# Performance work log

Hardware: AMD Instinct MI355X
Metric: run time of the kernel (lower is better)

## Reference

```python
import jax, jax.numpy as jnp
import numpy as np

N_NODES = 100000
N_EDGES = 1000000
N_GRAPHS = 5000
H = 64
F_IN = 14  # QM9 num_features (11) + pos (3)
BN_EPS = 1e-5


def setup_inputs() -> dict:
    key = jax.random.key(0)
    ks = jax.random.split(key, 16)

    def w(k, shape, fan_in):
        return (jax.random.normal(k, shape, jnp.float32) / np.sqrt(fan_in)).astype(jnp.float32)

    inp = {
        "x": jax.random.normal(ks[0], (N_NODES, 11), jnp.float32),
        "pos": jax.random.normal(ks[1], (N_NODES, 3), jnp.float32),
        "edge_index": jax.random.randint(ks[2], (2, N_EDGES), 0, N_NODES, dtype=jnp.int32),
        "batch": jnp.sort(jax.random.randint(ks[3], (N_NODES,), 0, N_GRAPHS, dtype=jnp.int32)),
    }
    dims = [F_IN, H, H]
    i = 4
    for l, din in enumerate(dims, 1):
        inp[f"w{l}a"] = w(ks[i], (din, H), din); i += 1
        inp[f"b{l}a"] = jnp.zeros((H,), jnp.float32)
        inp[f"g{l}"] = jnp.ones((H,), jnp.float32)   # BatchNorm gamma
        inp[f"be{l}"] = jnp.zeros((H,), jnp.float32)  # BatchNorm beta
        inp[f"w{l}b"] = w(ks[i], (H, H), H); i += 1
        inp[f"b{l}b"] = jnp.zeros((H,), jnp.float32)
    inp["wl1"] = w(ks[i], (3 * H, H), 3 * H); i += 1
    inp["bl1"] = jnp.zeros((H,), jnp.float32)
    inp["wl2"] = w(ks[i], (H, 1), H)
    inp["bl2"] = jnp.zeros((1,), jnp.float32)
    return inp


def _gin_layer(x, src, dst, w1, b1, g, be, w2, b2):
    # GINConv (eps=0): h = MLP(x + sum_{j in N(i)} x_j)
    agg = jax.ops.segment_sum(x[src], dst, num_segments=x.shape[0])
    h = (x + agg) @ w1 + b1
    # BatchNorm1d in training mode: batch stats over node dim (biased var)
    mu = jnp.mean(h, axis=0)
    var = jnp.mean((h - mu) ** 2, axis=0)
    h = jax.nn.relu(g * (h - mu) * jax.lax.rsqrt(var + BN_EPS) + be)
    return jax.nn.relu(h @ w2 + b2)


def _mean_pool(x, batch):
    s = jax.ops.segment_sum(x, batch, num_segments=N_GRAPHS)
    c = jax.ops.segment_sum(jnp.ones((x.shape[0], 1), x.dtype), batch, num_segments=N_GRAPHS)
    return s / jnp.maximum(c, 1.0)


def reference(x, pos, edge_index, batch,
              w1a, b1a, g1, be1, w1b, b1b,
              w2a, b2a, g2, be2, w2b, b2b,
              w3a, b3a, g3, be3, w3b, b3b,
              wl1, bl1, wl2, bl2):
    src, dst = edge_index[0], edge_index[1]
    h0 = jnp.concatenate([x, pos], axis=1)                 # [N, 14]
    x1 = _gin_layer(h0, src, dst, w1a, b1a, g1, be1, w1b, b1b)
    x2 = _gin_layer(x1, src, dst, w2a, b2a, g2, be2, w2b, b2b)
    x3 = _gin_layer(x2, src, dst, w3a, b3a, g3, be3, w3b, b3b)
    p = jnp.concatenate([_mean_pool(x1, batch), _mean_pool(x2, batch), _mean_pool(x3, batch)], axis=1)  # [G, 192]
    h = jax.nn.relu(p @ wl1 + bl1)
    return h @ wl2 + bl2                                   # [G, 1]
```

## Files before the change

### kernel.cpp

```cpp
#include <hip/hip_runtime.h>
#include <hip/hip_bf16.h>

#define BN_EPS 1e-5f
#define LDP 132
#define LDS_BF 72
#define BSH 9
#define EPB 4096

typedef short bf16x8 __attribute__((ext_vector_type(8)));
typedef float f32x4 __attribute__((ext_vector_type(4)));

__device__ __forceinline__ float loadf(const void* p, long long i, unsigned bf) {
    if (bf) return __bfloat162float(((const __hip_bfloat16*)p)[i]);
    return ((const float*)p)[i];
}
__device__ __forceinline__ float b2f(unsigned short u) {
    return __uint_as_float(((unsigned)u) << 16);
}
__device__ __forceinline__ unsigned short f2b(float f) {
    __hip_bfloat16 h = __float2bfloat16(f);
    return *(unsigned short*)&h;
}
__device__ __forceinline__ float blo(unsigned u) { return __uint_as_float(u << 16); }
__device__ __forceinline__ float bhi(unsigned u) { return __uint_as_float(u & 0xffff0000u); }

__global__ void k_detect(const unsigned* g1w, unsigned* flag) {
    if (threadIdx.x == 0) *flag = (*g1w == 0x3F803F80u) ? 1u : 0u;
}

struct Srcs { const void* p[22]; };

__global__ void k_convert(Srcs s, const unsigned* flag, float* dst) {
    const int sizes[22] = {896,64,64,64,4096,64,  4096,64,64,64,4096,64,
                           4096,64,64,64,4096,64, 12288,64,64,1};
    const int offs[22]  = {0,896,960,1024,1088,5184, 5248,9344,9408,9472,9536,13632,
                           13696,17792,17856,17920,17984,22080, 22144,34432,34496,34560};
    int t = blockIdx.x;
    unsigned bf = *flag;
    const void* src = s.p[t];
    float* d = dst + offs[t];
    int n = sizes[t];
    for (int i = threadIdx.x; i < n; i += blockDim.x) d[i] = loadf(src, i, bf);
}

__global__ __launch_bounds__(256) void k_build(const void* x, const void* pos, const int* batch,
                        const unsigned* flag, unsigned short* h0b, float* cnt, int N) {
    int i = blockIdx.x * blockDim.x + threadIdx.x;
    if (i >= N) return;
    unsigned bf = *flag;
    unsigned short v[16];
    #pragma unroll
    for (int k = 0; k < 11; k++) v[k] = f2b(loadf(x, (long long)i * 11 + k, bf));
    #pragma unroll
    for (int k = 0; k < 3; k++) v[11 + k] = f2b(loadf(pos, (long long)i * 3 + k, bf));
    v[14] = 0; v[15] = 0;
    #pragma unroll
    for (int k = 0; k < 4; k++)
        *(ushort4*)&h0b[(long long)i * 16 + k * 4] = make_ushort4(v[4*k], v[4*k+1], v[4*k+2], v[4*k+3]);
    atomicAdd(&cnt[batch[i]], 1.0f);
}

__global__ __launch_bounds__(256) void k_bhist(const int* __restrict__ ei, int* __restrict__ bcnt,
                                               int E, int NCH, int NBK) {
    __shared__ int h[1024];
    int c = blockIdx.x, t = threadIdx.x;
    for (int i = t; i < NBK; i += 256) h[i] = 0;
    __syncthreads();
    int base = c * EPB;
    for (int i = t; i < EPB; i += 256) {
        int e = base + i;
        if (e < E) atomicAdd(&h[ei[E + e] >> BSH], 1);
    }
    __syncthreads();
    for (int i = t; i < NBK; i += 256) bcnt[i * NCH + c] = h[i];
}

__global__ __launch_bounds__(256) void k_scan_partial(const int* __restrict__ src, int* partial, int M) {
    __shared__ int sr[4];
    int b = blockIdx.x, t = threadIdx.x;
    int base = b * 1024;
    int s = 0;
    #pragma unroll
    for (int k = 0; k < 4; k++) {
        int i = base + k * 256 + t;
        if (i < M) s += src[i];
    }
    #pragma unroll
    for (int off = 32; off; off >>= 1) s += __shfl_down(s, off);
    if ((t & 63) == 0) sr[t >> 6] = s;
    __syncthreads();
    if (t == 0) partial[b] = sr[0] + sr[1] + sr[2] + sr[3];
}

__global__ __launch_bounds__(1024) void k_scan_chunks(const int* partial, int* chunkoff, int nchunks) {
    __shared__ int sp[1024];
    int t = threadIdx.x;
    sp[t] = (t < nchunks) ? partial[t] : 0;
    __syncthreads();
    for (int off = 1; off < 1024; off <<= 1) {
        int v = (t >= off) ? sp[t - off] : 0;
        __syncthreads();
        sp[t] += v;
        __syncthreads();
    }
    if (t < nchunks) chunkoff[t] = (t == 0) ? 0 : sp[t - 1];
}

__global__ __launch_bounds__(256) void k_scan_final(const int* __restrict__ src, const int* chunkoff,
                                                    int* __restrict__ out, int M) {
    __shared__ int sp[256];
    int b = blockIdx.x, t = threadIdx.x;
    int base = b * 1024 + t * 4;
    int v0 = 0, v1 = 0, v2 = 0, v3 = 0;
    if (base + 0 < M) v0 = src[base + 0];
    if (base + 1 < M) v1 = src[base + 1];
    if (base + 2 < M) v2 = src[base + 2];
    if (base + 3 < M) v3 = src[base + 3];
    int s = v0 + v1 + v2 + v3;
    sp[t] = s;
    __syncthreads();
    for (int off = 1; off < 256; off <<= 1) {
        int v = (t >= off) ? sp[t - off] : 0;
        __syncthreads();
        sp[t] += v;
        __syncthreads();
    }
    int run = chunkoff[b] + sp[t] - s;
    if (base + 0 < M) { out[base + 0] = run; run += v0; }
    if (base + 1 < M) { out[base + 1] = run; run += v1; }
    if (base + 2 < M) { out[base + 2] = run; run += v2; }
    if (base + 3 < M) { out[base + 3] = run; }
}

__global__ __launch_bounds__(256) void k_place(const int* __restrict__ ei, const int* __restrict__ boff,
                                               int2* __restrict__ ebuf, int E, int NCH, int NBK) {
    __shared__ int cur[1024];
    int c = blockIdx.x, t = threadIdx.x;
    for (int i = t; i < NBK; i += 256) cur[i] = boff[i * NCH + c];
    __syncthreads();
    int base = c * EPB;
    for (int i = t; i < EPB; i += 256) {
        int e = base + i;
        if (e < E) {
            int s = ei[e], d = ei[E + e];
            int pos = atomicAdd(&cur[d >> BSH], 1);
            ebuf[pos] = make_int2(s, d);
        }
    }
}

__global__ __launch_bounds__(256) void k_bucket_fill(const int2* __restrict__ ebuf, const int* __restrict__ boff,
                                                     int* __restrict__ roff, int* __restrict__ csr,
                                                     int N, int E, int NCH, int NBK) {
    __shared__ int cnt[512];
    __shared__ int exc[512];
    __shared__ int curb[512];
    __shared__ int sp[256];
    int b = blockIdx.x, t = threadIdx.x;
    int d0 = b << BSH;
    int dpb = N - d0; if (dpb > 512) dpb = 512;
    int segS = boff[b * NCH];
    int segE = (b + 1 < NBK) ? boff[(b + 1) * NCH] : E;
    cnt[t] = 0; cnt[t + 256] = 0;
    __syncthreads();
    for (int k = segS + t; k < segE; k += 256) atomicAdd(&cnt[ebuf[k].y - d0], 1);
    __syncthreads();
    int a0 = cnt[2 * t], a1 = cnt[2 * t + 1];
    sp[t] = a0 + a1;
    __syncthreads();
    for (int off = 1; off < 256; off <<= 1) {
        int v = (t >= off) ? sp[t - off] : 0;
        __syncthreads();
        sp[t] += v;
        __syncthreads();
    }
    int pre = (t == 0) ? 0 : sp[t - 1];
    exc[2 * t] = pre; exc[2 * t + 1] = pre + a0;
    curb[2 * t] = pre; curb[2 * t + 1] = pre + a0;
    __syncthreads();
    for (int i = t; i < dpb; i += 256) roff[d0 + i] = segS + exc[i];
    if (b == NBK - 1 && t == 0) roff[N] = E;
    for (int k = segS + t; k < segE; k += 256) {
        int2 p = ebuf[k];
        int lp = atomicAdd(&curb[p.y - d0], 1);
        csr[segS + lp] = p.x;
    }
}

__global__ __launch_bounds__(256) void k_gmm_bn14(const int* __restrict__ roff, const int* __restrict__ csr,
        const unsigned short* __restrict__ h0b, const float* __restrict__ W,
        const float* __restrict__ bias, unsigned short* __restrict__ Hb,
        float* bnsum, float* bnsumsq, int N) {
    __shared__ float sA[14 * LDP];
    __shared__ float sW[14 * 64];
    __shared__ float sRs[4 * 64];
    __shared__ float sRq[4 * 64];
    int tid = threadIdx.x;
    int row0 = blockIdx.x * 128;
    int rows = N - row0; if (rows > 128) rows = 128;
    for (int i = tid; i < 14 * 64; i += 256) sW[i] = W[i];
    const unsigned* h0u = (const unsigned*)h0b;
    int q = tid & 7, nn = tid >> 3;
    #pragma unroll
    for (int it = 0; it < 4; it++) {
        int r = nn + it * 32;
        float a0 = 0.f, a1 = 0.f;
        if (r < rows) {
            int gr = row0 + r;
            unsigned su = h0u[(long long)gr * 8 + q];
            a0 = blo(su); a1 = bhi(su);
            int e0 = roff[gr], e1 = roff[gr + 1];
            int k = e0;
            float b0 = 0.f, b1 = 0.f;
            for (; k + 1 < e1; k += 2) {
                unsigned u0 = h0u[(long long)csr[k] * 8 + q];
                unsigned u1 = h0u[(long long)csr[k + 1] * 8 + q];
                a0 += blo(u0); a1 += bhi(u0);
                b0 += blo(u1); b1 += bhi(u1);
            }
            if (k < e1) {
                unsigned u0 = h0u[(long long)csr[k] * 8 + q];
                a0 += blo(u0); a1 += bhi(u0);
            }
            a0 += b0; a1 += b1;
        }
        if (2 * q < 14)     sA[(2 * q) * LDP + r] = a0;
        if (2 * q + 1 < 14) sA[(2 * q + 1) * LDP + r] = a1;
    }
    __syncthreads();
    int tx = tid & 15, ty = tid >> 4;
    float4 bj = *(const float4*)&bias[tx * 4];
    float acc[8][4];
    #pragma unroll
    for (int i = 0; i < 8; i++) { acc[i][0] = bj.x; acc[i][1] = bj.y; acc[i][2] = bj.z; acc[i][3] = bj.w; }
    #pragma unroll
    for (int k = 0; k < 14; k++) {
        const float4 a0 = *(const float4*)&sA[k * LDP + ty * 8];
        const float4 a1 = *(const float4*)&sA[k * LDP + ty * 8 + 4];
        const float4 w  = *(const float4*)&sW[k * 64 + tx * 4];
        const float av[8] = {a0.x, a0.y, a0.z, a0.w, a1.x, a1.y, a1.z, a1.w};
        #pragma unroll
        for (int i = 0; i < 8; i++) {
            acc[i][0] += av[i] * w.x; acc[i][1] += av[i] * w.y;
            acc[i][2] += av[i] * w.z; acc[i][3] += av[i] * w.w;
        }
    }
    float cs[4] = {0.f, 0.f, 0.f, 0.f}, cq[4] = {0.f, 0.f, 0.f, 0.f};
    #pragma unroll
    for (int i = 0; i < 8; i++) {
        int r = ty * 8 + i;
        if (r < rows) {
            int gr = row0 + r;
            ushort4 hv;
            hv.x = f2b(acc[i][0]); hv.y = f2b(acc[i][1]);
            hv.z = f2b(acc[i][2]); hv.w = f2b(acc[i][3]);
            *(ushort4*)&Hb[(long long)gr * 64 + tx * 4] = hv;
            #pragma unroll
            for (int d = 0; d < 4; d++) { cs[d] += acc[i][d]; cq[d] += acc[i][d] * acc[i][d]; }
        }
    }
    #pragma unroll
    for (int d = 0; d < 4; d++) {
        cs[d] += __shfl_xor(cs[d], 16); cs[d] += __shfl_xor(cs[d], 32);
        cq[d] += __shfl_xor(cq[d], 16); cq[d] += __shfl_xor(cq[d], 32);
    }
    int wid = tid >> 6, lane = tid & 63;
    if (lane < 16) {
        #pragma unroll
        for (int d = 0; d < 4; d++) {
            sRs[wid * 64 + lane * 4 + d] = cs[d];
            sRq[wid * 64 + lane * 4 + d] = cq[d];
        }
    }
    __syncthreads();
    if (tid < 64) atomicAdd(&bnsum[tid], sRs[tid] + sRs[64 + tid] + sRs[128 + tid] + sRs[192 + tid]);
    else if (tid < 128) {
        int j = tid - 64;
        atomicAdd(&bnsumsq[j], sRq[j] + sRq[64 + j] + sRq[128 + j] + sRq[192 + j]);
    }
}

__global__ __launch_bounds__(256) void k_gmm_bn64(const int* __restrict__ roff, const int* __restrict__ csr,
        const unsigned short* __restrict__ xinb, const float* __restrict__ W,
        const float* __restrict__ bias, unsigned short* __restrict__ Hb,
        float* bnsum, float* bnsumsq, int N) {
    __shared__ unsigned short sS[128 * LDS_BF];
    __shared__ unsigned short sWt[64 * LDS_BF];
    __shared__ float sRs[4 * 64];
    __shared__ float sRq[4 * 64];
    int tid = threadIdx.x;
    int row0 = blockIdx.x * 128;
    int rows = N - row0; if (rows > 128) rows = 128;
    for (int i = tid; i < 4096; i += 256) {
        int k = i >> 6, n = i & 63;
        sWt[n * LDS_BF + k] = f2b(W[i]);
    }
    const ushort4* xr = (const ushort4*)xinb;
    int q = tid & 15, nn = tid >> 4;
    #pragma unroll
    for (int it = 0; it < 8; it++) {
        int r = nn + it * 16;
        float4 acc = make_float4(0.f, 0.f, 0.f, 0.f);
        if (r < rows) {
            int gr = row0 + r;
            ushort4 u = xr[(long long)gr * 16 + q];
            acc = make_float4(b2f(u.x), b2f(u.y), b2f(u.z), b2f(u.w));
            float4 acc2 = make_float4(0.f, 0.f, 0.f, 0.f);
            int e0 = roff[gr], e1 = roff[gr + 1];
            int k = e0;
            for (; k + 1 < e1; k += 2) {
                int s0 = csr[k], s1 = csr[k + 1];
                ushort4 v0 = xr[(long long)s0 * 16 + q];
                ushort4 v1 = xr[(long long)s1 * 16 + q];
                acc.x += b2f(v0.x); acc.y += b2f(v0.y); acc.z += b2f(v0.z); acc.w += b2f(v0.w);
                acc2.x += b2f(v1.x); acc2.y += b2f(v1.y); acc2.z += b2f(v1.z); acc2.w += b2f(v1.w);
            }
            if (k < e1) {
                int s0 = csr[k];
                ushort4 v0 = xr[(long long)s0 * 16 + q];
                acc.x += b2f(v0.x); acc.y += b2f(v0.y); acc.z += b2f(v0.z); acc.w += b2f(v0.w);
            }
            acc.x += acc2.x; acc.y += acc2.y; acc.z += acc2.z; acc.w += acc2.w;
        }
        ushort4 o;
        o.x = f2b(acc.x); o.y = f2b(acc.y); o.z = f2b(acc.z); o.w = f2b(acc.w);
        *(ushort4*)&sS[r * LDS_BF + q * 4] = o;
    }
    __syncthreads();
    int w = tid >> 6, lane = tid & 63;
    int half = lane >> 4, m = lane & 15;
    f32x4 acc[2][4];
    #pragma unroll
    for (int rt = 0; rt < 2; rt++)
        #pragma unroll
        for (int ct = 0; ct < 4; ct++) acc[rt][ct] = (f32x4){0.f, 0.f, 0.f, 0.f};
    #pragma unroll
    for (int km = 0; km < 2; km++) {
        bf16x8 a0 = *(const bf16x8*)&sS[(w * 32 + m) * LDS_BF + km * 32 + half * 8];
        bf16x8 a1 = *(const bf16x8*)&sS[(w * 32 + 16 + m) * LDS_BF + km * 32 + half * 8];
        #pragma unroll
        for (int ct = 0; ct < 4; ct++) {
            bf16x8 b = *(const bf16x8*)&sWt[(ct * 16 + m) * LDS_BF + km * 32 + half * 8];
            acc[0][ct] = __builtin_amdgcn_mfma_f32_16x16x32_bf16(a0, b, acc[0][ct], 0, 0, 0);
            acc[1][ct] = __builtin_amdgcn_mfma_f32_16x16x32_bf16(a1, b, acc[1][ct], 0, 0, 0);
        }
    }
    float cs[4] = {0.f, 0.f, 0.f, 0.f}, cq[4] = {0.f, 0.f, 0.f, 0.f};
    #pragma unroll
    for (int ct = 0; ct < 4; ct++) {
        float bj = bias[ct * 16 + m];
        #pragma unroll
        for (int rt = 0; rt < 2; rt++) {
            #pragma unroll
            for (int r = 0; r < 4; r++) {
                int lr = w * 32 + rt * 16 + half * 4 + r;
                if (lr < rows) {
                    float v = acc[rt][ct][r] + bj;
                    Hb[(long long)(row0 + lr) * 64 + ct * 16 + m] = f2b(v);
                    cs[ct] += v; cq[ct] += v * v;
                }
            }
        }
    }
    #pragma unroll
    for (int d = 0; d < 4; d++) {
        cs[d] += __shfl_xor(cs[d], 16); cs[d] += __shfl_xor(cs[d], 32);
        cq[d] += __shfl_xor(cq[d], 16); cq[d] += __shfl_xor(cq[d], 32);
    }
    if (lane < 16) {
        #pragma unroll
        for (int ct = 0; ct < 4; ct++) {
            sRs[w * 64 + ct * 16 + lane] = cs[ct];
            sRq[w * 64 + ct * 16 + lane] = cq[ct];
        }
    }
    __syncthreads();
    if (tid < 64) atomicAdd(&bnsum[tid], sRs[tid] + sRs[64 + tid] + sRs[128 + tid] + sRs[192 + tid]);
    else if (tid < 128) {
        int j = tid - 64;
        atomicAdd(&bnsumsq[j], sRq[j] + sRq[64 + j] + sRq[128 + j] + sRq[192 + j]);
    }
}

__global__ __launch_bounds__(256) void k_bn_mm2_rt(const unsigned short* __restrict__ Hb, const float* __restrict__ g,
        const float* __restrict__ be, const float* __restrict__ W2, const float* __restrict__ b2,
        const float* bnsum, const float* bnsumsq, const int* __restrict__ batch,
        unsigned short* __restrict__ xout, float* pool, int N, float invN, int loff) {
    __shared__ unsigned short sS[128 * LDS_BF];
    __shared__ unsigned short sWt[64 * LDS_BF];
    __shared__ float sSc[64];
    __shared__ float sSh[64];
    int tid = threadIdx.x;
    int row0 = blockIdx.x * 128;
    int rows = N - row0; if (rows > 128) rows = 128;
    if (tid < 64) {
        float mu = bnsum[tid] * invN;
        float var = bnsumsq[tid] * invN - mu * mu;
        float sc = g[tid] * rsqrtf(var + BN_EPS);
        sSc[tid] = sc; sSh[tid] = be[tid] - sc * mu;
    }
    for (int i = tid; i < 4096; i += 256) {
        int k = i >> 6, n = i & 63;
        sWt[n * LDS_BF + k] = f2b(W2[i]);
    }
    __syncthreads();
    #pragma unroll
    for (int it = 0; it < 8; it++) {
        int idx = tid + it * 256;
        int r = idx >> 4, q = idx & 15;
        ushort4 o = make_ushort4(0, 0, 0, 0);
        if (r < rows) {
            ushort4 u = *(const ushort4*)&Hb[(long long)(row0 + r) * 64 + (q << 2)];
            o.x = f2b(fmaxf(sSc[q*4+0] * b2f(u.x) + sSh[q*4+0], 0.f));
            o.y = f2b(fmaxf(sSc[q*4+1] * b2f(u.y) + sSh[q*4+1], 0.f));
            o.z = f2b(fmaxf(sSc[q*4+2] * b2f(u.z) + sSh[q*4+2], 0.f));
            o.w = f2b(fmaxf(sSc[q*4+3] * b2f(u.w) + sSh[q*4+3], 0.f));
        }
        *(ushort4*)&sS[r * LDS_BF + q * 4] = o;
    }
    __syncthreads();
    int w = tid >> 6, lane = tid & 63;
    int half = lane >> 4, m = lane & 15;
    f32x4 acc[2][4];
    #pragma unroll
    for (int rt = 0; rt < 2; rt++)
        #pragma unroll
        for (int ct = 0; ct < 4; ct++) acc[rt][ct] = (f32x4){0.f, 0.f, 0.f, 0.f};
    #pragma unroll
    for (int km = 0; km < 2; km++) {
        bf16x8 a0 = *(const bf16x8*)&sS[(w * 32 + m) * LDS_BF + km * 32 + half * 8];
        bf16x8 a1 = *(const bf16x8*)&sS[(w * 32 + 16 + m) * LDS_BF + km * 32 + half * 8];
        #pragma unroll
        for (int ct = 0; ct < 4; ct++) {
            bf16x8 b = *(const bf16x8*)&sWt[(ct * 16 + m) * LDS_BF + km * 32 + half * 8];
            acc[0][ct] = __builtin_amdgcn_mfma_f32_16x16x32_bf16(a0, b, acc[0][ct], 0, 0, 0);
            acc[1][ct] = __builtin_amdgcn_mfma_f32_16x16x32_bf16(a1, b, acc[1][ct], 0, 0, 0);
        }
    }
    float b2j[4];
    #pragma unroll
    for (int ct = 0; ct < 4; ct++) b2j[ct] = b2[ct * 16 + m];
    int prevg = -1;
    float p[4] = {0.f, 0.f, 0.f, 0.f};
    #pragma unroll
    for (int rt = 0; rt < 2; rt++) {
        #pragma unroll
        for (int r = 0; r < 4; r++) {
            int lr = w * 32 + rt * 16 + half * 4 + r;
            if (lr < rows) {
                int gr = row0 + lr;
                float o[4];
                #pragma unroll
                for (int ct = 0; ct < 4; ct++) {
                    o[ct] = fmaxf(acc[rt][ct][r] + b2j[ct], 0.f);
                    if (xout) xout[(long long)gr * 64 + ct * 16 + m] = f2b(o[ct]);
                }
                int gid = batch[gr];
                if (gid != prevg) {
                    if (prevg >= 0) {
                        float* pp = &pool[(long long)prevg * 192 + loff + m];
                        atomicAdd(pp + 0,  p[0]); atomicAdd(pp + 16, p[1]);
                        atomicAdd(pp + 32, p[2]); atomicAdd(pp + 48, p[3]);
                    }
                    prevg = gid;
                    p[0] = o[0]; p[1] = o[1]; p[2] = o[2]; p[3] = o[3];
                } else {
                    p[0] += o[0]; p[1] += o[1]; p[2] += o[2]; p[3] += o[3];
                }
            }
        }
    }
    if (prevg >= 0) {
        float* pp = &pool[(long long)prevg * 192 + loff + m];
        atomicAdd(pp + 0,  p[0]); atomicAdd(pp + 16, p[1]);
        atomicAdd(pp + 32, p[2]); atomicAdd(pp + 48, p[3]);
    }
}

__global__ __launch_bounds__(64) void k_head(const float* pool, const float* cnt,
                        const float* wl1, const float* bl1, const float* wl2, const float* bl2,
                        const unsigned* flag, void* out, int G) {
    int gb = blockIdx.x; int j = threadIdx.x;
    if (gb >= G) return;
    __shared__ float sP[192];
    float c = fmaxf(cnt[gb], 1.0f);
    float inv = 1.0f / c;
    for (int k = j; k < 192; k += 64) sP[k] = pool[(long long)gb * 192 + k] * inv;
    __syncthreads();
    float acc = bl1[j];
    for (int k = 0; k < 192; k++) acc += sP[k] * wl1[k * 64 + j];
    float v = fmaxf(acc, 0.f) * wl2[j];
    #pragma unroll
    for (int off = 32; off; off >>= 1) v += __shfl_down(v, off);
    if (j == 0) {
        float res = v + bl2[0];
        if (*flag) ((__hip_bfloat16*)out)[gb] = __float2bfloat16(res);
        else       ((float*)out)[gb] = res;
    }
}

extern "C" void kernel_launch(void* const* d_in, const int* in_sizes, int n_in,
                              void* d_out, int out_size, void* d_ws, size_t ws_size,
                              hipStream_t stream) {
    const void* x   = d_in[0];
    const void* pos = d_in[1];
    const int* ei    = (const int*)d_in[2];
    const int* batch = (const int*)d_in[3];
    const int N = in_sizes[3];
    const int E = in_sizes[2] / 2;
    const int G = out_size;

    float* ws = (float*)d_ws;
    unsigned* flag = (unsigned*)ws;
    float* P = ws + 16;
    float* w1a = P + 0;     float* b1a = P + 896;   float* g1 = P + 960;   float* be1 = P + 1024;
    float* w1b = P + 1088;  float* b1b = P + 5184;
    float* w2a = P + 5248;  float* b2a = P + 9344;  float* g2 = P + 9408;  float* be2 = P + 9472;
    float* w2b = P + 9536;  float* b2b = P + 13632;
    float* w3a = P + 13696; float* b3a = P + 17792; float* g3 = P + 17856; float* be3 = P + 17920;
    float* w3b = P + 17984; float* b3b = P + 22080;
    float* wl1 = P + 22144; float* bl1 = P + 34432; float* wl2 = P + 34496; float* bl2 = P + 34560;

    long long off = 16 + 34592;
    float* h0r  = ws + off;                 off += (long long)N * 14;
    float* aggr = ws + off;                 off += (long long)N * 64;
    float* Hbuf = ws + off;                 off += (long long)N * 64;
    float* curf = ws + off;                 off += (long long)N * 64;
    float* pool = ws + off;                 off += (long long)G * 192;
    float* cnt  = ws + off;                 off += G;
    float* bn   = ws + off;                 off += 128;
    int*   roff = (int*)(ws + off);
    int* csr = roff + (N + 1);

    unsigned short* h0b  = (unsigned short*)h0r;
    unsigned short* curh = (unsigned short*)curf;
    unsigned short* Hh   = (unsigned short*)Hbuf;

    const int NBK = (N + 511) >> BSH;
    const int NCH = (E + EPB - 1) / EPB;
    const int M = NBK * NCH;
    int* bcnt     = csr + E;
    int* boff     = bcnt + M;
    int* partial  = boff + M;
    int* chunkoff = partial + 1024;
    int2* ebuf = (int2*)Hbuf;

    hipMemsetAsync(pool, 0, ((size_t)G * 192 + (size_t)G) * sizeof(float), stream);

    k_detect<<<1, 1, 0, stream>>>((const unsigned*)d_in[6], flag);

    Srcs s;
    for (int i = 0; i < 22; i++) s.p[i] = d_in[4 + i];
    k_convert<<<22, 256, 0, stream>>>(s, flag, P);

    int nb = (N + 255) / 256;
    k_build<<<nb, 256, 0, stream>>>(x, pos, batch, flag, h0b, cnt, N);

    k_bhist<<<NCH, 256, 0, stream>>>(ei, bcnt, E, NCH, NBK);
    int nchS = (M + 1023) / 1024;
    k_scan_partial<<<nchS, 256, 0, stream>>>(bcnt, partial, M);
    k_scan_chunks<<<1, 1024, 0, stream>>>(partial, chunkoff, nchS);
    k_scan_final<<<nchS, 256, 0, stream>>>(bcnt, chunkoff, boff, M);
    k_place<<<NCH, 256, 0, stream>>>(ei, boff, ebuf, E, NCH, NBK);
    k_bucket_fill<<<NBK, 256, 0, stream>>>(ebuf, boff, roff, csr, N, E, NCH, NBK);

    int rtBlocks = (N + 127) / 128;
    float invN = 1.0f / (float)N;

    hipMemsetAsync(bn, 0, 128 * sizeof(float), stream);
    k_gmm_bn14<<<rtBlocks, 256, 0, stream>>>(roff, csr, h0b, w1a, b1a, Hh, bn, bn + 64, N);
    k_bn_mm2_rt<<<rtBlocks, 256, 0, stream>>>(Hh, g1, be1, w1b, b1b, bn, bn + 64, batch,
                                              curh, pool, N, invN, 0);
    hipMemsetAsync(bn, 0, 128 * sizeof(float), stream);
    k_gmm_bn64<<<rtBlocks, 256, 0, stream>>>(roff, csr, curh, w2a, b2a, Hh, bn, bn + 64, N);
    k_bn_mm2_rt<<<rtBlocks, 256, 0, stream>>>(Hh, g2, be2, w2b, b2b, bn, bn + 64, batch,
                                              curh, pool, N, invN, 64);
    hipMemsetAsync(bn, 0, 128 * sizeof(float), stream);
    k_gmm_bn64<<<rtBlocks, 256, 0, stream>>>(roff, csr, curh, w3a, b3a, Hh, bn, bn + 64, N);
    k_bn_mm2_rt<<<rtBlocks, 256, 0, stream>>>(Hh, g3, be3, w3b, b3b, bn, bn + 64, batch,
                                              nullptr, pool, N, invN, 128);

    k_head<<<G, 64, 0, stream>>>(pool, cnt, wl1, bl1, wl2, bl2, flag, d_out, G);
}
```

Measured before the change: 393.1 us.

## Split 64-wide neighbor gather out of fused gather-matmul into separate kernel

Layers 2 and 3 previously ran the CSR neighbor aggregation inside the matmul+BN-stats kernel, with 128 rows per block and a 2-way unrolled edge loop. The aggregation now runs in its own kernel with one 16-lane group per node, 16 nodes per block and a 4-way unrolled edge loop, and writes a bf16 aggregate buffer that the matmul kernel then loads. The aim is more blocks in flight and more loads outstanding per lane for the latency-bound random gather. The cost is an extra bf16 N×64 write and read through global memory, plus one more launch per layer.

Result: faster. 375.7 us (-4.4%).

```diff
diff --git a/kernel.cpp b/kernel.cpp
--- a/kernel.cpp
+++ b/kernel.cpp
@@ -280,8 +280,45 @@
     }
 }
 
-__global__ __launch_bounds__(256) void k_gmm_bn64(const int* __restrict__ roff, const int* __restrict__ csr,
-        const unsigned short* __restrict__ xinb, const float* __restrict__ W,
+__global__ __launch_bounds__(256) void k_gather64(const int* __restrict__ roff, const int* __restrict__ csr,
+                                                  const unsigned short* __restrict__ xinb,
+                                                  unsigned short* __restrict__ aggb, int N) {
+    int g = threadIdx.x >> 4, q = threadIdx.x & 15;
+    int node = blockIdx.x * 16 + g;
+    if (node >= N) return;
+    const ushort4* xr = (const ushort4*)xinb;
+    ushort4 u = xr[(long long)node * 16 + q];
+    float4 a0 = make_float4(b2f(u.x), b2f(u.y), b2f(u.z), b2f(u.w));
+    float4 a1 = make_float4(0.f, 0.f, 0.f, 0.f);
+    float4 a2 = make_float4(0.f, 0.f, 0.f, 0.f);
+    float4 a3 = make_float4(0.f, 0.f, 0.f, 0.f);
+    int e0 = roff[node], e1 = roff[node + 1];
+    int k = e0;
+    for (; k + 3 < e1; k += 4) {
+        int s0 = csr[k], s1 = csr[k + 1], s2 = csr[k + 2], s3 = csr[k + 3];
+        ushort4 v0 = xr[(long long)s0 * 16 + q];
+        ushort4 v1 = xr[(long long)s1 * 16 + q];
+        ushort4 v2 = xr[(long long)s2 * 16 + q];
+        ushort4 v3 = xr[(long long)s3 * 16 + q];
+        a0.x += b2f(v0.x); a0.y += b2f(v0.y); a0.z += b2f(v0.z); a0.w += b2f(v0.w);
+        a1.x += b2f(v1.x); a1.y += b2f(v1.y); a1.z += b2f(v1.z); a1.w += b2f(v1.w);
+        a2.x += b2f(v2.x); a2.y += b2f(v2.y); a2.z += b2f(v2.z); a2.w += b2f(v2.w);
+        a3.x += b2f(v3.x); a3.y += b2f(v3.y); a3.z += b2f(v3.z); a3.w += b2f(v3.w);
+    }
+    for (; k < e1; k++) {
+        ushort4 v0 = xr[(long long)csr[k] * 16 + q];
+        a0.x += b2f(v0.x); a0.y += b2f(v0.y); a0.z += b2f(v0.z); a0.w += b2f(v0.w);
+    }
+    a0.x += a1.x + a2.x + a3.x;
+    a0.y += a1.y + a2.y + a3.y;
+    a0.z += a1.z + a2.z + a3.z;
+    a0.w += a1.w + a2.w + a3.w;
+    ushort4 o;
+    o.x = f2b(a0.x); o.y = f2b(a0.y); o.z = f2b(a0.z); o.w = f2b(a0.w);
+    *(ushort4*)&aggb[(long long)node * 64 + q * 4] = o;
+}
+
+__global__ __launch_bounds__(256) void k_mm_bn64(const unsigned short* __restrict__ Sb, const float* __restrict__ W,
         const float* __restrict__ bias, unsigned short* __restrict__ Hb,
         float* bnsum, float* bnsumsq, int N) {
     __shared__ unsigned short sS[128 * LDS_BF];
@@ -291,40 +328,17 @@
     int tid = threadIdx.x;
     int row0 = blockIdx.x * 128;
     int rows = N - row0; if (rows > 128) rows = 128;
+    #pragma unroll
+    for (int it = 0; it < 8; it++) {
+        int idx = tid + it * 256;
+        int r = idx >> 4, q = idx & 15;
+        ushort4 v = make_ushort4(0, 0, 0, 0);
+        if (r < rows) v = *(const ushort4*)&Sb[(long long)(row0 + r) * 64 + (q << 2)];
+        *(ushort4*)&sS[r * LDS_BF + q * 4] = v;
+    }
     for (int i = tid; i < 4096; i += 256) {
         int k = i >> 6, n = i & 63;
         sWt[n * LDS_BF + k] = f2b(W[i]);
-    }
-    const ushort4* xr = (const ushort4*)xinb;
-    int q = tid & 15, nn = tid >> 4;
-    #pragma unroll
-    for (int it = 0; it < 8; it++) {
-        int r = nn + it * 16;
-        float4 acc = make_float4(0.f, 0.f, 0.f, 0.f);
-        if (r < rows) {
-            int gr = row0 + r;
-            ushort4 u = xr[(long long)gr * 16 + q];
-            acc = make_float4(b2f(u.x), b2f(u.y), b2f(u.z), b2f(u.w));
-            float4 acc2 = make_float4(0.f, 0.f, 0.f, 0.f);
-            int e0 = roff[gr], e1 = roff[gr + 1];
-            int k = e0;
-            for (; k + 1 < e1; k += 2) {
-                int s0 = csr[k], s1 = csr[k + 1];
-                ushort4 v0 = xr[(long long)s0 * 16 + q];
-                ushort4 v1 = xr[(long long)s1 * 16 + q];
-                acc.x += b2f(v0.x); acc.y += b2f(v0.y); acc.z += b2f(v0.z); acc.w += b2f(v0.w);
-                acc2.x += b2f(v1.x); acc2.y += b2f(v1.y); acc2.z += b2f(v1.z); acc2.w += b2f(v1.w);
-            }
-            if (k < e1) {
-                int s0 = csr[k];
-                ushort4 v0 = xr[(long long)s0 * 16 + q];
-                acc.x += b2f(v0.x); acc.y += b2f(v0.y); acc.z += b2f(v0.z); acc.w += b2f(v0.w);
-            }
-            acc.x += acc2.x; acc.y += acc2.y; acc.z += acc2.z; acc.w += acc2.w;
-        }
-        ushort4 o;
-        o.x = f2b(acc.x); o.y = f2b(acc.y); o.z = f2b(acc.z); o.w = f2b(acc.w);
-        *(ushort4*)&sS[r * LDS_BF + q * 4] = o;
     }
     __syncthreads();
     int w = tid >> 6, lane = tid & 63;
@@ -533,6 +547,7 @@
     int* csr = roff + (N + 1);
 
     unsigned short* h0b  = (unsigned short*)h0r;
+    unsigned short* aggh = (unsigned short*)aggr;
     unsigned short* curh = (unsigned short*)curf;
     unsigned short* Hh   = (unsigned short*)Hbuf;
 
@@ -565,18 +580,21 @@
     k_bucket_fill<<<NBK, 256, 0, stream>>>(ebuf, boff, roff, csr, N, E, NCH, NBK);
 
     int rtBlocks = (N + 127) / 128;
+    int gBlocks = (N + 15) / 16;
     float invN = 1.0f / (float)N;
 
     hipMemsetAsync(bn, 0, 128 * sizeof(float), stream);
     k_gmm_bn14<<<rtBlocks, 256, 0, stream>>>(roff, csr, h0b, w1a, b1a, Hh, bn, bn + 64, N);
     k_bn_mm2_rt<<<rtBlocks, 256, 0, stream>>>(Hh, g1, be1, w1b, b1b, bn, bn + 64, batch,
                                               curh, pool, N, invN, 0);
+    k_gather64<<<gBlocks, 256, 0, stream>>>(roff, csr, curh, aggh, N);
     hipMemsetAsync(bn, 0, 128 * sizeof(float), stream);
-    k_gmm_bn64<<<rtBlocks, 256, 0, stream>>>(roff, csr, curh, w2a, b2a, Hh, bn, bn + 64, N);
+    k_mm_bn64<<<rtBlocks, 256, 0, stream>>>(aggh, w2a, b2a, Hh, bn, bn + 64, N);
     k_bn_mm2_rt<<<rtBlocks, 256, 0, stream>>>(Hh, g2, be2, w2b, b2b, bn, bn + 64, batch,
                                               curh, pool, N, invN, 64);
+    k_gather64<<<gBlocks, 256, 0, stream>>>(roff, csr, curh, aggh, N);
     hipMemsetAsync(bn, 0, 128 * sizeof(float), stream);
-    k_gmm_bn64<<<rtBlocks, 256, 0, stream>>>(roff, csr, curh, w3a, b3a, Hh, bn, bn + 64, N);
+    k_mm_bn64<<<rtBlocks, 256, 0, stream>>>(aggh, w3a, b3a, Hh, bn, bn + 64, N);
     k_bn_mm2_rt<<<rtBlocks, 256, 0, stream>>>(Hh, g3, be3, w3b, b3b, bn, bn + 64, batch,
                                               nullptr, pool, N, invN, 128);
 
```
